# Performance work log

Measured on AMD Instinct MI355X. Metric: run time of the kernel, lower is better.

The kernel has to match this reference:

```python
import jax, jax.numpy as jnp
import numpy as np

D_MODEL = 1024
N_HEAD = 16
D_HEAD = D_MODEL // N_HEAD


def setup_inputs() -> dict:
    key = jax.random.key(0)
    k_x, k_qkv, k_proj = jax.random.split(key, 3)
    B, T = 2, 2048
    x = jax.random.normal(k_x, (B, T, D_MODEL), dtype=jnp.float32)
    # torch Linear weight [out, in]; y = x @ W.T. Scale ~ kaiming-uniform-ish.
    s = 1.0 / np.sqrt(D_MODEL)
    W_qkv = jax.random.uniform(k_qkv, (3 * D_MODEL, D_MODEL), dtype=jnp.float32, minval=-s, maxval=s)
    W_proj = jax.random.uniform(k_proj, (D_MODEL, D_MODEL), dtype=jnp.float32, minval=-s, maxval=s)
    return {"x": x, "W_qkv": W_qkv, "W_proj": W_proj}


def reference(x, W_qkv, W_proj):
    B, T, C = x.shape
    qkv = jnp.einsum('btc,oc->bto', x, W_qkv)  # [B,T,3C]
    q, k, v = jnp.split(qkv, 3, axis=-1)
    # [B,T,C] -> [B,H,T,Dh]
    def heads(t):
        return t.reshape(B, T, N_HEAD, D_HEAD).transpose(0, 2, 1, 3)
    q, k, v = heads(q), heads(k), heads(v)
    scale = 1.0 / np.sqrt(D_HEAD)
    scores = jnp.einsum('bhqd,bhkd->bhqk', q, k) * scale  # [B,H,T,T]
    causal = jnp.tril(jnp.ones((T, T), dtype=bool))
    scores = jnp.where(causal, scores, jnp.finfo(scores.dtype).min)
    attn = jax.nn.softmax(scores, axis=-1)
    y = jnp.einsum('bhqk,bhkd->bhqd', attn, v)  # [B,H,T,Dh]
    y = y.transpose(0, 2, 1, 3).reshape(B, T, C)
    return jnp.einsum('btc,oc->bto', y, W_proj)
```

## Files before the change

### kernel.cpp

```cpp
#include <hip/hip_runtime.h>

typedef unsigned short u16;
typedef float f32x4 __attribute__((ext_vector_type(4)));
typedef __bf16 bf16x8 __attribute__((ext_vector_type(8)));
typedef unsigned int u32x4 __attribute__((ext_vector_type(4)));
typedef u16 u16x4 __attribute__((ext_vector_type(4)));
typedef u16 u16x8 __attribute__((ext_vector_type(8)));

static __device__ __forceinline__ u16 f2bf(float f) {
  union { __bf16 h; u16 u; } c;
  c.h = (__bf16)f;
  return c.u;
}

static __device__ __forceinline__ void gload_lds16(const void* g, void* l) {
  __builtin_amdgcn_global_load_lds(
      (const __attribute__((address_space(1))) unsigned int*)g,
      (__attribute__((address_space(3))) unsigned int*)l, 16, 0, 0);
}

__global__ __launch_bounds__(256) void cvt_f32_bf16(const float* __restrict__ in,
                                                    u16* __restrict__ out, int n4) {
  int i = blockIdx.x * 256 + threadIdx.x;
  if (i < n4) {
    f32x4 v = *((const f32x4*)in + i);
    u16x4 o;
    o[0] = f2bf(v[0]); o[1] = f2bf(v[1]); o[2] = f2bf(v[2]); o[3] = f2bf(v[3]);
    *((u16x4*)out + i) = o;
  }
}

template<int OUT_BF16>
__global__ __launch_bounds__(256) void gemm_nt(const u16* __restrict__ A,
                                               const u16* __restrict__ B,
                                               void* __restrict__ Cp,
                                               int M, int N, int K) {
  __shared__ __align__(16) u16 lA[128 * 64];
  __shared__ __align__(16) u16 lB[128 * 64];
  const int tid = threadIdx.x;
  const int lane = tid & 63;
  const int wave = tid >> 6;
  const int wm = wave >> 1, wn = wave & 1;
  const int l15 = lane & 15, lg = lane >> 4;
  const int bm = blockIdx.y * 128, bn = blockIdx.x * 128;

  f32x4 acc[4][4];
#pragma unroll
  for (int i = 0; i < 4; ++i)
#pragma unroll
    for (int j = 0; j < 4; ++j) acc[i][j] = (f32x4){0.f, 0.f, 0.f, 0.f};

  const u16* Ag[4];
  const u16* Bg[4];
#pragma unroll
  for (int it = 0; it < 4; ++it) {
    const int s = it * 256 + tid;
    const int row = s >> 3, g = s & 7;
    const int gsw = g ^ (row & 7);
    Ag[it] = A + (size_t)(bm + row) * K + gsw * 8;
    Bg[it] = B + (size_t)(bn + row) * K + gsw * 8;
  }

  for (int k0 = 0; k0 < K; k0 += 64) {
#pragma unroll
    for (int it = 0; it < 4; ++it) {
      gload_lds16(Ag[it] + k0, (u16*)lA + (size_t)(it * 256 + tid) * 8);
      gload_lds16(Bg[it] + k0, (u16*)lB + (size_t)(it * 256 + tid) * 8);
    }
    __syncthreads();
#pragma unroll
    for (int kk = 0; kk < 2; ++kk) {
      bf16x8 af[4], bfv[4];
#pragma unroll
      for (int mf = 0; mf < 4; ++mf) {
        const int row = wm * 64 + mf * 16 + l15;
        af[mf] = *(const bf16x8*)((const char*)lA + row * 128 +
                                  ((kk * 64 + lg * 16) ^ ((row & 7) << 4)));
      }
#pragma unroll
      for (int nf = 0; nf < 4; ++nf) {
        const int row = wn * 64 + nf * 16 + l15;
        bfv[nf] = *(const bf16x8*)((const char*)lB + row * 128 +
                                   ((kk * 64 + lg * 16) ^ ((row & 7) << 4)));
      }
#pragma unroll
      for (int mf = 0; mf < 4; ++mf)
#pragma unroll
        for (int nf = 0; nf < 4; ++nf)
          acc[mf][nf] = __builtin_amdgcn_mfma_f32_16x16x32_bf16(af[mf], bfv[nf], acc[mf][nf], 0, 0, 0);
    }
    __syncthreads();
  }

#pragma unroll
  for (int mf = 0; mf < 4; ++mf) {
#pragma unroll
    for (int r = 0; r < 4; ++r) {
      const int row = bm + wm * 64 + mf * 16 + lg * 4 + r;
#pragma unroll
      for (int nf = 0; nf < 4; ++nf) {
        const int col = bn + wn * 64 + nf * 16 + l15;
        const float v = acc[mf][nf][r];
        if (OUT_BF16) ((u16*)Cp)[(size_t)row * N + col] = f2bf(v);
        else          ((float*)Cp)[(size_t)row * N + col] = v;
      }
    }
  }
}

__global__ __launch_bounds__(256) void transpose_v(const u16* __restrict__ qkv,
                                                   u16* __restrict__ vt) {
  constexpr int T = 2048, C3 = 3072, D = 64;
  __shared__ u16 lt[64 * 65];
  const int t0 = blockIdx.x * 64;
  const int bh = blockIdx.y;
  const int b = bh >> 4, h = bh & 15;
  const int tid = threadIdx.x;
#pragma unroll
  for (int it = 0; it < 2; ++it) {
    const int c = tid + it * 256;
    const int tr = c >> 3, d0 = (c & 7) * 8;
    u32x4 v = *(const u32x4*)&qkv[((size_t)b * T + t0 + tr) * C3 + 2048 + h * D + d0];
    const u16* pv = (const u16*)&v;
#pragma unroll
    for (int e = 0; e < 8; ++e) lt[tr * 65 + d0 + e] = pv[e];
  }
  __syncthreads();
#pragma unroll
  for (int it = 0; it < 2; ++it) {
    const int c = tid + it * 256;
    const int d = c >> 3, toff = (c & 7) * 8;
    u16x8 tmp;
#pragma unroll
    for (int e = 0; e < 8; ++e) tmp[e] = lt[(toff + e) * 65 + d];
    *(u16x8*)&vt[((size_t)bh * D + d) * T + t0 + toff] = tmp;
  }
}

__global__ __launch_bounds__(256) void attn_fwd(const u16* __restrict__ qkv,
                                                const u16* __restrict__ vt,
                                                u16* __restrict__ y) {
  constexpr int T = 2048, C = 1024, C3 = 3072, D = 64, NQ = 32;
  __shared__ __align__(16) u16 lK[2][64 * 64];
  __shared__ __align__(16) u16 lV[2][64 * 64];
  __shared__ __align__(16) u16 lP[4 * 16 * 64];
  const int tid = threadIdx.x, lane = tid & 63, w = tid >> 6;
  const int l15 = lane & 15, lg = lane >> 4;

  const int bid = blockIdx.x;
  const int xcd = bid & 7, slot = bid >> 3;
  const int bh = xcd * 4 + (slot >> 4);
  const int pi = slot & 15;
  const int b = bh >> 4, h = bh & 15;

  const int r0 = tid >> 3, off0 = (tid & 7) * 8;
  const int r1 = (tid + 256) >> 3, off1 = off0;
  const int sb0 = (off0 * 2) ^ ((r0 & 7) << 4);
  const int sb1 = (off1 * 2) ^ ((r1 & 7) << 4);
  const u16* Kbase = qkv + (size_t)b * T * C3 + C + h * D;
  const u16* Vbase = vt + (size_t)bh * D * T;

  const float qscale = 0.125f * 1.44269504088896f;

#pragma unroll 1
  for (int qi = 0; qi < 2; ++qi) {
    const int qt = (qi == 0) ? pi : (NQ - 1 - pi);
    const int q0 = qt * 64;

    const size_t qoff = ((size_t)b * T + q0 + w * 16 + l15) * C3 + h * D;
    const bf16x8 aq0 = *(const bf16x8*)&qkv[qoff + lg * 8];
    const bf16x8 aq1 = *(const bf16x8*)&qkv[qoff + 32 + lg * 8];

    float m = -1.0e30f, l = 0.f;
    f32x4 o_acc[4];
#pragma unroll
    for (int nf = 0; nf < 4; ++nf) o_acc[nf] = (f32x4){0.f, 0.f, 0.f, 0.f};

    u32x4 rk0 = *(const u32x4*)(Kbase + (size_t)r0 * C3 + off0);
    u32x4 rk1 = *(const u32x4*)(Kbase + (size_t)r1 * C3 + off1);
    u32x4 rv0 = *(const u32x4*)(Vbase + (size_t)r0 * T + off0);
    u32x4 rv1 = *(const u32x4*)(Vbase + (size_t)r1 * T + off1);
    __syncthreads();
    *(u32x4*)&lK[0][(r0 * 128 + sb0) >> 1] = rk0;
    *(u32x4*)&lK[0][(r1 * 128 + sb1) >> 1] = rk1;
    *(u32x4*)&lV[0][(r0 * 128 + sb0) >> 1] = rv0;
    *(u32x4*)&lV[0][(r1 * 128 + sb1) >> 1] = rv1;
    if (qt > 0) {
      rk0 = *(const u32x4*)(Kbase + (size_t)(64 + r0) * C3 + off0);
      rk1 = *(const u32x4*)(Kbase + (size_t)(64 + r1) * C3 + off1);
      rv0 = *(const u32x4*)(Vbase + (size_t)r0 * T + 64 + off0);
      rv1 = *(const u32x4*)(Vbase + (size_t)r1 * T + 64 + off1);
    }

    for (int kt = 0; kt <= qt; ++kt) {
      const int cur = kt & 1;
      __syncthreads();
      if (kt < qt) {
        *(u32x4*)&lK[cur ^ 1][(r0 * 128 + sb0) >> 1] = rk0;
        *(u32x4*)&lK[cur ^ 1][(r1 * 128 + sb1) >> 1] = rk1;
        *(u32x4*)&lV[cur ^ 1][(r0 * 128 + sb0) >> 1] = rv0;
        *(u32x4*)&lV[cur ^ 1][(r1 * 128 + sb1) >> 1] = rv1;
        if (kt + 1 < qt) {
          const int kn = (kt + 2) * 64;
          rk0 = *(const u32x4*)(Kbase + (size_t)(kn + r0) * C3 + off0);
          rk1 = *(const u32x4*)(Kbase + (size_t)(kn + r1) * C3 + off1);
          rv0 = *(const u32x4*)(Vbase + (size_t)r0 * T + kn + off0);
          rv1 = *(const u32x4*)(Vbase + (size_t)r1 * T + kn + off1);
        }
      }
      const u16* Kc = lK[cur];
      const u16* Vc = lV[cur];

      f32x4 s[4];
#pragma unroll
      for (int nf = 0; nf < 4; ++nf) s[nf] = (f32x4){0.f, 0.f, 0.f, 0.f};
      __builtin_amdgcn_s_setprio(1);
#pragma unroll
      for (int nf = 0; nf < 4; ++nf) {
        const int row = nf * 16 + l15;
        const int x = (row & 7) << 4;
        bf16x8 bk0 = *(const bf16x8*)&Kc[(row * 128 + ((lg * 16) ^ x)) >> 1];
        bf16x8 bk1 = *(const bf16x8*)&Kc[(row * 128 + ((64 + lg * 16) ^ x)) >> 1];
        s[nf] = __builtin_amdgcn_mfma_f32_16x16x32_bf16(bk0, aq0, s[nf], 0, 0, 0);
        s[nf] = __builtin_amdgcn_mfma_f32_16x16x32_bf16(bk1, aq1, s[nf], 0, 0, 0);
      }
      __builtin_amdgcn_s_setprio(0);

#pragma unroll
      for (int nf = 0; nf < 4; ++nf) {
#pragma unroll
        for (int r = 0; r < 4; ++r) {
          float v = s[nf][r] * qscale;
          if (kt == qt) {
            if (nf * 16 + lg * 4 + r > w * 16 + l15) v = -1.0e30f;
          }
          s[nf][r] = v;
        }
      }

      float t0a = fmaxf(fmaxf(s[0][0], s[0][1]), fmaxf(s[0][2], s[0][3]));
      float t1a = fmaxf(fmaxf(s[1][0], s[1][1]), fmaxf(s[1][2], s[1][3]));
      float t2a = fmaxf(fmaxf(s[2][0], s[2][1]), fmaxf(s[2][2], s[2][3]));
      float t3a = fmaxf(fmaxf(s[3][0], s[3][1]), fmaxf(s[3][2], s[3][3]));
      float pmax = fmaxf(fmaxf(t0a, t1a), fmaxf(t2a, t3a));
      pmax = fmaxf(pmax, __shfl_xor(pmax, 16));
      pmax = fmaxf(pmax, __shfl_xor(pmax, 32));

      if (!__all(pmax <= m)) {
        const float mnew = fmaxf(m, pmax);
        const float fct = __builtin_amdgcn_exp2f(m - mnew);
        m = mnew;
        l *= fct;
#pragma unroll
        for (int r = 0; r < 4; ++r) {
          const float fr = __shfl(fct, lg * 4 + r);
#pragma unroll
          for (int nf = 0; nf < 4; ++nf) o_acc[nf][r] *= fr;
        }
      }

      float p[4][4];
#pragma unroll
      for (int nf = 0; nf < 4; ++nf)
#pragma unroll
        for (int r = 0; r < 4; ++r) p[nf][r] = __builtin_amdgcn_exp2f(s[nf][r] - m);
      float s0a = (p[0][0] + p[0][1]) + (p[0][2] + p[0][3]);
      float s1a = (p[1][0] + p[1][1]) + (p[1][2] + p[1][3]);
      float s2a = (p[2][0] + p[2][1]) + (p[2][2] + p[2][3]);
      float s3a = (p[3][0] + p[3][1]) + (p[3][2] + p[3][3]);
      float psum = (s0a + s1a) + (s2a + s3a);
      psum += __shfl_xor(psum, 16);
      psum += __shfl_xor(psum, 32);
      l += psum;

#pragma unroll
      for (int nf = 0; nf < 4; ++nf) {
        u16x4 pk;
        pk[0] = f2bf(p[nf][0]); pk[1] = f2bf(p[nf][1]);
        pk[2] = f2bf(p[nf][2]); pk[3] = f2bf(p[nf][3]);
        *(u16x4*)&lP[(w * 2048 + l15 * 128 + ((nf * 32 + lg * 8) ^ ((l15 & 7) << 4))) >> 1] = pk;
      }

      __builtin_amdgcn_s_setprio(1);
#pragma unroll
      for (int sj = 0; sj < 2; ++sj) {
        bf16x8 ap = *(const bf16x8*)&lP[(w * 2048 + l15 * 128 + ((sj * 64 + lg * 16) ^ ((l15 & 7) << 4))) >> 1];
#pragma unroll
        for (int nf = 0; nf < 4; ++nf) {
          const int d = nf * 16 + l15;
          bf16x8 bv = *(const bf16x8*)&Vc[(d * 128 + ((sj * 64 + lg * 16) ^ ((d & 7) << 4))) >> 1];
          o_acc[nf] = __builtin_amdgcn_mfma_f32_16x16x32_bf16(ap, bv, o_acc[nf], 0, 0, 0);
        }
      }
      __builtin_amdgcn_s_setprio(0);
    }

#pragma unroll
    for (int r = 0; r < 4; ++r) {
      const float li = __builtin_amdgcn_rcpf(__shfl(l, lg * 4 + r));
      const int row = q0 + w * 16 + lg * 4 + r;
#pragma unroll
      for (int nf = 0; nf < 4; ++nf) {
        const int col = h * D + nf * 16 + l15;
        y[((size_t)b * T + row) * C + col] = f2bf(o_acc[nf][r] * li);
      }
    }
  }
}

extern "C" void kernel_launch(void* const* d_in, const int* in_sizes, int n_in,
                              void* d_out, int out_size, void* d_ws, size_t ws_size,
                              hipStream_t stream) {
  const float* x = (const float*)d_in[0];
  const float* Wqkv = (const float*)d_in[1];
  const float* Wproj = (const float*)d_in[2];
  float* out = (float*)d_out;

  constexpr int B = 2, T = 2048, C = 1024, C3 = 3072, H = 16, D = 64;
  constexpr int M = B * T;

  u16* xb = (u16*)d_ws;
  u16* wqkvb = xb + (size_t)M * C;
  u16* wprojb = wqkvb + (size_t)C3 * C;
  u16* qkvb = wprojb + (size_t)C * C;
  u16* vtb = qkvb + (size_t)M * C3;
  u16* yb = vtb + (size_t)M * C;

  cvt_f32_bf16<<<dim3((M * C) / 4 / 256), 256, 0, stream>>>(x, xb, (M * C) / 4);
  cvt_f32_bf16<<<dim3((C3 * C) / 4 / 256), 256, 0, stream>>>(Wqkv, wqkvb, (C3 * C) / 4);
  cvt_f32_bf16<<<dim3((C * C) / 4 / 256), 256, 0, stream>>>(Wproj, wprojb, (C * C) / 4);

  gemm_nt<1><<<dim3(C3 / 128, M / 128), 256, 0, stream>>>(xb, wqkvb, qkvb, M, C3, C);
  transpose_v<<<dim3(T / 64, B * H), 256, 0, stream>>>(qkvb, vtb);
  attn_fwd<<<dim3(512), 256, 0, stream>>>(qkvb, vtb, yb);
  gemm_nt<0><<<dim3(C / 128, M / 128), 256, 0, stream>>>(yb, wprojb, out, M, C, C);
}
```

Before: 118.5 us.

## Process paired query tiles concurrently sharing each K/V tile load

Instead of running the short and long query tiles of a causal pair one after another, each block now processes both tiles in a single KV loop. Each K/V tile staged in LDS is used by both query tiles while the short tile is still active, which removes the second pass of K/V loads and its barriers. The block-to-head mapping is also changed so the second half of the blocks takes the pair indices in reverse order. The cost is roughly double the accumulator and score registers, a second P buffer in LDS, and a launch_bounds occupancy hint of 2 that may force register spills.

```diff
diff --git a/kernel.cpp b/kernel.cpp
--- a/kernel.cpp
+++ b/kernel.cpp
@@ -137,21 +137,70 @@
   }
 }
 
-__global__ __launch_bounds__(256) void attn_fwd(const u16* __restrict__ qkv,
-                                                const u16* __restrict__ vt,
-                                                u16* __restrict__ y) {
+static __device__ __forceinline__ void online_sm(f32x4 (&s)[4], bool diag,
+                                                 int lg, int l15, int w,
+                                                 float qscale, float& m, float& l,
+                                                 f32x4 (&o)[4]) {
+  const int ql = w * 16 + l15;
+#pragma unroll
+  for (int nf = 0; nf < 4; ++nf)
+#pragma unroll
+    for (int r = 0; r < 4; ++r) {
+      float v = s[nf][r] * qscale;
+      if (diag && (nf * 16 + lg * 4 + r > ql)) v = -1.0e30f;
+      s[nf][r] = v;
+    }
+  float t0a = fmaxf(fmaxf(s[0][0], s[0][1]), fmaxf(s[0][2], s[0][3]));
+  float t1a = fmaxf(fmaxf(s[1][0], s[1][1]), fmaxf(s[1][2], s[1][3]));
+  float t2a = fmaxf(fmaxf(s[2][0], s[2][1]), fmaxf(s[2][2], s[2][3]));
+  float t3a = fmaxf(fmaxf(s[3][0], s[3][1]), fmaxf(s[3][2], s[3][3]));
+  float pmax = fmaxf(fmaxf(t0a, t1a), fmaxf(t2a, t3a));
+  pmax = fmaxf(pmax, __shfl_xor(pmax, 16));
+  pmax = fmaxf(pmax, __shfl_xor(pmax, 32));
+  if (!__all(pmax <= m)) {
+    const float mnew = fmaxf(m, pmax);
+    const float fct = __builtin_amdgcn_exp2f(m - mnew);
+    m = mnew;
+    l *= fct;
+#pragma unroll
+    for (int r = 0; r < 4; ++r) {
+      const float fr = __shfl(fct, lg * 4 + r);
+#pragma unroll
+      for (int nf = 0; nf < 4; ++nf) o[nf][r] *= fr;
+    }
+  }
+#pragma unroll
+  for (int nf = 0; nf < 4; ++nf)
+#pragma unroll
+    for (int r = 0; r < 4; ++r) s[nf][r] = __builtin_amdgcn_exp2f(s[nf][r] - m);
+  float s0a = (s[0][0] + s[0][1]) + (s[0][2] + s[0][3]);
+  float s1a = (s[1][0] + s[1][1]) + (s[1][2] + s[1][3]);
+  float s2a = (s[2][0] + s[2][1]) + (s[2][2] + s[2][3]);
+  float s3a = (s[3][0] + s[3][1]) + (s[3][2] + s[3][3]);
+  float psum = (s0a + s1a) + (s2a + s3a);
+  psum += __shfl_xor(psum, 16);
+  psum += __shfl_xor(psum, 32);
+  l += psum;
+}
+
+__global__ __launch_bounds__(256, 2) void attn_fwd(const u16* __restrict__ qkv,
+                                                   const u16* __restrict__ vt,
+                                                   u16* __restrict__ y) {
   constexpr int T = 2048, C = 1024, C3 = 3072, D = 64, NQ = 32;
   __shared__ __align__(16) u16 lK[2][64 * 64];
   __shared__ __align__(16) u16 lV[2][64 * 64];
-  __shared__ __align__(16) u16 lP[4 * 16 * 64];
+  __shared__ __align__(16) u16 lP[2][4 * 16 * 64];
   const int tid = threadIdx.x, lane = tid & 63, w = tid >> 6;
   const int l15 = lane & 15, lg = lane >> 4;
 
   const int bid = blockIdx.x;
   const int xcd = bid & 7, slot = bid >> 3;
-  const int bh = xcd * 4 + (slot >> 4);
-  const int pi = slot & 15;
+  const int half = slot >> 5, s5 = slot & 31;
+  const int bh = xcd * 4 + (s5 >> 4) + 2 * half;
+  const int pp = s5 & 15;
+  const int pi = half ? (15 - pp) : pp;
   const int b = bh >> 4, h = bh & 15;
+  const int qa = pi, qb = NQ - 1 - pi;
 
   const int r0 = tid >> 3, off0 = (tid & 7) * 8;
   const int r1 = (tid + 256) >> 3, off1 = off0;
@@ -162,148 +211,127 @@
 
   const float qscale = 0.125f * 1.44269504088896f;
 
-#pragma unroll 1
-  for (int qi = 0; qi < 2; ++qi) {
-    const int qt = (qi == 0) ? pi : (NQ - 1 - pi);
-    const int q0 = qt * 64;
-
-    const size_t qoff = ((size_t)b * T + q0 + w * 16 + l15) * C3 + h * D;
-    const bf16x8 aq0 = *(const bf16x8*)&qkv[qoff + lg * 8];
-    const bf16x8 aq1 = *(const bf16x8*)&qkv[qoff + 32 + lg * 8];
-
-    float m = -1.0e30f, l = 0.f;
-    f32x4 o_acc[4];
-#pragma unroll
-    for (int nf = 0; nf < 4; ++nf) o_acc[nf] = (f32x4){0.f, 0.f, 0.f, 0.f};
-
-    u32x4 rk0 = *(const u32x4*)(Kbase + (size_t)r0 * C3 + off0);
-    u32x4 rk1 = *(const u32x4*)(Kbase + (size_t)r1 * C3 + off1);
-    u32x4 rv0 = *(const u32x4*)(Vbase + (size_t)r0 * T + off0);
-    u32x4 rv1 = *(const u32x4*)(Vbase + (size_t)r1 * T + off1);
+  const size_t qoffA = ((size_t)b * T + qa * 64 + w * 16 + l15) * C3 + h * D;
+  const size_t qoffB = ((size_t)b * T + qb * 64 + w * 16 + l15) * C3 + h * D;
+  const bf16x8 aqA0 = *(const bf16x8*)&qkv[qoffA + lg * 8];
+  const bf16x8 aqA1 = *(const bf16x8*)&qkv[qoffA + 32 + lg * 8];
+  const bf16x8 aqB0 = *(const bf16x8*)&qkv[qoffB + lg * 8];
+  const bf16x8 aqB1 = *(const bf16x8*)&qkv[qoffB + 32 + lg * 8];
+
+  float mA = -1.0e30f, lA2 = 0.f, mB = -1.0e30f, lB2 = 0.f;
+  f32x4 oA[4], oB[4];
+#pragma unroll
+  for (int nf = 0; nf < 4; ++nf) {
+    oA[nf] = (f32x4){0.f, 0.f, 0.f, 0.f};
+    oB[nf] = (f32x4){0.f, 0.f, 0.f, 0.f};
+  }
+
+  u32x4 rk0 = *(const u32x4*)(Kbase + (size_t)r0 * C3 + off0);
+  u32x4 rk1 = *(const u32x4*)(Kbase + (size_t)r1 * C3 + off1);
+  u32x4 rv0 = *(const u32x4*)(Vbase + (size_t)r0 * T + off0);
+  u32x4 rv1 = *(const u32x4*)(Vbase + (size_t)r1 * T + off1);
+  *(u32x4*)&lK[0][(r0 * 128 + sb0) >> 1] = rk0;
+  *(u32x4*)&lK[0][(r1 * 128 + sb1) >> 1] = rk1;
+  *(u32x4*)&lV[0][(r0 * 128 + sb0) >> 1] = rv0;
+  *(u32x4*)&lV[0][(r1 * 128 + sb1) >> 1] = rv1;
+  rk0 = *(const u32x4*)(Kbase + (size_t)(64 + r0) * C3 + off0);
+  rk1 = *(const u32x4*)(Kbase + (size_t)(64 + r1) * C3 + off1);
+  rv0 = *(const u32x4*)(Vbase + (size_t)r0 * T + 64 + off0);
+  rv1 = *(const u32x4*)(Vbase + (size_t)r1 * T + 64 + off1);
+
+  for (int kt = 0; kt <= qb; ++kt) {
+    const int cur = kt & 1;
     __syncthreads();
-    *(u32x4*)&lK[0][(r0 * 128 + sb0) >> 1] = rk0;
-    *(u32x4*)&lK[0][(r1 * 128 + sb1) >> 1] = rk1;
-    *(u32x4*)&lV[0][(r0 * 128 + sb0) >> 1] = rv0;
-    *(u32x4*)&lV[0][(r1 * 128 + sb1) >> 1] = rv1;
-    if (qt > 0) {
-      rk0 = *(const u32x4*)(Kbase + (size_t)(64 + r0) * C3 + off0);
-      rk1 = *(const u32x4*)(Kbase + (size_t)(64 + r1) * C3 + off1);
-      rv0 = *(const u32x4*)(Vbase + (size_t)r0 * T + 64 + off0);
-      rv1 = *(const u32x4*)(Vbase + (size_t)r1 * T + 64 + off1);
-    }
-
-    for (int kt = 0; kt <= qt; ++kt) {
-      const int cur = kt & 1;
-      __syncthreads();
-      if (kt < qt) {
-        *(u32x4*)&lK[cur ^ 1][(r0 * 128 + sb0) >> 1] = rk0;
-        *(u32x4*)&lK[cur ^ 1][(r1 * 128 + sb1) >> 1] = rk1;
-        *(u32x4*)&lV[cur ^ 1][(r0 * 128 + sb0) >> 1] = rv0;
-        *(u32x4*)&lV[cur ^ 1][(r1 * 128 + sb1) >> 1] = rv1;
-        if (kt + 1 < qt) {
-          const int kn = (kt + 2) * 64;
-          rk0 = *(const u32x4*)(Kbase + (size_t)(kn + r0) * C3 + off0);
-          rk1 = *(const u32x4*)(Kbase + (size_t)(kn + r1) * C3 + off1);
-          rv0 = *(const u32x4*)(Vbase + (size_t)r0 * T + kn + off0);
-          rv1 = *(const u32x4*)(Vbase + (size_t)r1 * T + kn + off1);
-        }
-      }
-      const u16* Kc = lK[cur];
-      const u16* Vc = lV[cur];
-
-      f32x4 s[4];
-#pragma unroll
-      for (int nf = 0; nf < 4; ++nf) s[nf] = (f32x4){0.f, 0.f, 0.f, 0.f};
-      __builtin_amdgcn_s_setprio(1);
-#pragma unroll
-      for (int nf = 0; nf < 4; ++nf) {
-        const int row = nf * 16 + l15;
-        const int x = (row & 7) << 4;
-        bf16x8 bk0 = *(const bf16x8*)&Kc[(row * 128 + ((lg * 16) ^ x)) >> 1];
-        bf16x8 bk1 = *(const bf16x8*)&Kc[(row * 128 + ((64 + lg * 16) ^ x)) >> 1];
-        s[nf] = __builtin_amdgcn_mfma_f32_16x16x32_bf16(bk0, aq0, s[nf], 0, 0, 0);
-        s[nf] = __builtin_amdgcn_mfma_f32_16x16x32_bf16(bk1, aq1, s[nf], 0, 0, 0);
-      }
-      __builtin_amdgcn_s_setprio(0);
-
-#pragma unroll
-      for (int nf = 0; nf < 4; ++nf) {
-#pragma unroll
-        for (int r = 0; r < 4; ++r) {
-          float v = s[nf][r] * qscale;
-          if (kt == qt) {
-            if (nf * 16 + lg * 4 + r > w * 16 + l15) v = -1.0e30f;
-          }
-          s[nf][r] = v;
-        }
-      }
-
-      float t0a = fmaxf(fmaxf(s[0][0], s[0][1]), fmaxf(s[0][2], s[0][3]));
-      float t1a = fmaxf(fmaxf(s[1][0], s[1][1]), fmaxf(s[1][2], s[1][3]));
-      float t2a = fmaxf(fmaxf(s[2][0], s[2][1]), fmaxf(s[2][2], s[2][3]));
-      float t3a = fmaxf(fmaxf(s[3][0], s[3][1]), fmaxf(s[3][2], s[3][3]));
-      float pmax = fmaxf(fmaxf(t0a, t1a), fmaxf(t2a, t3a));
-      pmax = fmaxf(pmax, __shfl_xor(pmax, 16));
-      pmax = fmaxf(pmax, __shfl_xor(pmax, 32));
-
-      if (!__all(pmax <= m)) {
-        const float mnew = fmaxf(m, pmax);
-        const float fct = __builtin_amdgcn_exp2f(m - mnew);
-        m = mnew;
-        l *= fct;
-#pragma unroll
-        for (int r = 0; r < 4; ++r) {
-          const float fr = __shfl(fct, lg * 4 + r);
-#pragma unroll
-          for (int nf = 0; nf < 4; ++nf) o_acc[nf][r] *= fr;
-        }
-      }
-
-      float p[4][4];
-#pragma unroll
-      for (int nf = 0; nf < 4; ++nf)
-#pragma unroll
-        for (int r = 0; r < 4; ++r) p[nf][r] = __builtin_amdgcn_exp2f(s[nf][r] - m);
-      float s0a = (p[0][0] + p[0][1]) + (p[0][2] + p[0][3]);
-      float s1a = (p[1][0] + p[1][1]) + (p[1][2] + p[1][3]);
-      float s2a = (p[2][0] + p[2][1]) + (p[2][2] + p[2][3]);
-      float s3a = (p[3][0] + p[3][1]) + (p[3][2] + p[3][3]);
-      float psum = (s0a + s1a) + (s2a + s3a);
-      psum += __shfl_xor(psum, 16);
-      psum += __shfl_xor(psum, 32);
-      l += psum;
-
+    if (kt < qb) {
+      *(u32x4*)&lK[cur ^ 1][(r0 * 128 + sb0) >> 1] = rk0;
+      *(u32x4*)&lK[cur ^ 1][(r1 * 128 + sb1) >> 1] = rk1;
+      *(u32x4*)&lV[cur ^ 1][(r0 * 128 + sb0) >> 1] = rv0;
+      *(u32x4*)&lV[cur ^ 1][(r1 * 128 + sb1) >> 1] = rv1;
+      if (kt + 1 < qb) {
+        const int kn = (kt + 2) * 64;
+        rk0 = *(const u32x4*)(Kbase + (size_t)(kn + r0) * C3 + off0);
+        rk1 = *(const u32x4*)(Kbase + (size_t)(kn + r1) * C3 + off1);
+        rv0 = *(const u32x4*)(Vbase + (size_t)r0 * T + kn + off0);
+        rv1 = *(const u32x4*)(Vbase + (size_t)r1 * T + kn + off1);
+      }
+    }
+    const u16* Kc = lK[cur];
+    const u16* Vc = lV[cur];
+    const bool actA = (kt <= qa);
+
+    f32x4 sA[4], sB[4];
+#pragma unroll
+    for (int nf = 0; nf < 4; ++nf) sB[nf] = (f32x4){0.f, 0.f, 0.f, 0.f};
+    if (actA) {
+#pragma unroll
+      for (int nf = 0; nf < 4; ++nf) sA[nf] = (f32x4){0.f, 0.f, 0.f, 0.f};
+    }
+    __builtin_amdgcn_s_setprio(1);
+#pragma unroll
+    for (int nf = 0; nf < 4; ++nf) {
+      const int row = nf * 16 + l15;
+      const int x = (row & 7) << 4;
+      bf16x8 bk0 = *(const bf16x8*)&Kc[(row * 128 + ((lg * 16) ^ x)) >> 1];
+      bf16x8 bk1 = *(const bf16x8*)&Kc[(row * 128 + ((64 + lg * 16) ^ x)) >> 1];
+      sB[nf] = __builtin_amdgcn_mfma_f32_16x16x32_bf16(bk0, aqB0, sB[nf], 0, 0, 0);
+      sB[nf] = __builtin_amdgcn_mfma_f32_16x16x32_bf16(bk1, aqB1, sB[nf], 0, 0, 0);
+      if (actA) {
+        sA[nf] = __builtin_amdgcn_mfma_f32_16x16x32_bf16(bk0, aqA0, sA[nf], 0, 0, 0);
+        sA[nf] = __builtin_amdgcn_mfma_f32_16x16x32_bf16(bk1, aqA1, sA[nf], 0, 0, 0);
+      }
+    }
+    __builtin_amdgcn_s_setprio(0);
+
+    online_sm(sB, kt == qb, lg, l15, w, qscale, mB, lB2, oB);
+    if (actA) online_sm(sA, kt == qa, lg, l15, w, qscale, mA, lA2, oA);
+
+    char* lPB = (char*)lP[1] + w * 2048;
+    char* lPA = (char*)lP[0] + w * 2048;
+#pragma unroll
+    for (int nf = 0; nf < 4; ++nf) {
+      u16x4 pk;
+      pk[0] = f2bf(sB[nf][0]); pk[1] = f2bf(sB[nf][1]);
+      pk[2] = f2bf(sB[nf][2]); pk[3] = f2bf(sB[nf][3]);
+      *(u16x4*)(lPB + l15 * 128 + ((nf * 32 + lg * 8) ^ ((l15 & 7) << 4))) = pk;
+    }
+    if (actA) {
 #pragma unroll
       for (int nf = 0; nf < 4; ++nf) {
         u16x4 pk;
-        pk[0] = f2bf(p[nf][0]); pk[1] = f2bf(p[nf][1]);
-        pk[2] = f2bf(p[nf][2]); pk[3] = f2bf(p[nf][3]);
-        *(u16x4*)&lP[(w * 2048 + l15 * 128 + ((nf * 32 + lg * 8) ^ ((l15 & 7) << 4))) >> 1] = pk;
-      }
-
-      __builtin_amdgcn_s_setprio(1);
-#pragma unroll
-      for (int sj = 0; sj < 2; ++sj) {
-        bf16x8 ap = *(const bf16x8*)&lP[(w * 2048 + l15 * 128 + ((sj * 64 + lg * 16) ^ ((l15 & 7) << 4))) >> 1];
-#pragma unroll
-        for (int nf = 0; nf < 4; ++nf) {
-          const int d = nf * 16 + l15;
-          bf16x8 bv = *(const bf16x8*)&Vc[(d * 128 + ((sj * 64 + lg * 16) ^ ((d & 7) << 4))) >> 1];
-          o_acc[nf] = __builtin_amdgcn_mfma_f32_16x16x32_bf16(ap, bv, o_acc[nf], 0, 0, 0);
-        }
-      }
-      __builtin_amdgcn_s_setprio(0);
-    }
-
-#pragma unroll
-    for (int r = 0; r < 4; ++r) {
-      const float li = __builtin_amdgcn_rcpf(__shfl(l, lg * 4 + r));
-      const int row = q0 + w * 16 + lg * 4 + r;
+        pk[0] = f2bf(sA[nf][0]); pk[1] = f2bf(sA[nf][1]);
+        pk[2] = f2bf(sA[nf][2]); pk[3] = f2bf(sA[nf][3]);
+        *(u16x4*)(lPA + l15 * 128 + ((nf * 32 + lg * 8) ^ ((l15 & 7) << 4))) = pk;
+      }
+    }
+
+    __builtin_amdgcn_s_setprio(1);
+#pragma unroll
+    for (int sj = 0; sj < 2; ++sj) {
+      bf16x8 apB = *(const bf16x8*)(lPB + l15 * 128 + ((sj * 64 + lg * 16) ^ ((l15 & 7) << 4)));
+      bf16x8 apA;
+      if (actA) apA = *(const bf16x8*)(lPA + l15 * 128 + ((sj * 64 + lg * 16) ^ ((l15 & 7) << 4)));
 #pragma unroll
       for (int nf = 0; nf < 4; ++nf) {
-        const int col = h * D + nf * 16 + l15;
-        y[((size_t)b * T + row) * C + col] = f2bf(o_acc[nf][r] * li);
-      }
+        const int d = nf * 16 + l15;
+        bf16x8 bv = *(const bf16x8*)&Vc[(d * 128 + ((sj * 64 + lg * 16) ^ ((d & 7) << 4))) >> 1];
+        oB[nf] = __builtin_amdgcn_mfma_f32_16x16x32_bf16(apB, bv, oB[nf], 0, 0, 0);
+        if (actA) oA[nf] = __builtin_amdgcn_mfma_f32_16x16x32_bf16(apA, bv, oA[nf], 0, 0, 0);
+      }
+    }
+    __builtin_amdgcn_s_setprio(0);
+  }
+
+#pragma unroll
+  for (int r = 0; r < 4; ++r) {
+    const float liA = __builtin_amdgcn_rcpf(__shfl(lA2, lg * 4 + r));
+    const float liB = __builtin_amdgcn_rcpf(__shfl(lB2, lg * 4 + r));
+    const int rowA = qa * 64 + w * 16 + lg * 4 + r;
+    const int rowB = qb * 64 + w * 16 + lg * 4 + r;
+#pragma unroll
+    for (int nf = 0; nf < 4; ++nf) {
+      const int col = h * D + nf * 16 + l15;
+      y[((size_t)b * T + rowA) * C + col] = f2bf(oA[nf][r] * liA);
+      y[((size_t)b * T + rowB) * C + col] = f2bf(oB[nf][r] * liB);
     }
   }
 }
```

Measured after the change: 127.4 us. +7.5%, slower.
